# Kernel tuning notes

Hardware: AMD Instinct MI355X
Metric: run time of the kernel (lower is better)

## Reference

```python
import jax, jax.numpy as jnp
import numpy as np

NH = 16      # query heads
NKV = 8      # kv heads
D = 128      # head_dim
HID = 2048   # hidden_size
EPS = 1e-6
THETA = 1e6


def _rmsnorm(x, w, eps=EPS):
    # x: [..., D]; per-head RMSNorm as in Qwen3 q_norm/k_norm
    var = jnp.mean(x * x, axis=-1, keepdims=True)
    return x * jax.lax.rsqrt(var + eps) * w


def _rope(positions, x, theta=THETA):
    # neox-style rotary (sglang get_rope default), rotary_dim == head_dim
    # x: [T, H, D]
    half = D // 2
    inv_freq = 1.0 / (theta ** (jnp.arange(half, dtype=jnp.float32) / half))
    ang = positions.astype(jnp.float32)[:, None] * inv_freq[None, :]   # [T, half]
    cos = jnp.cos(ang)[:, None, :]
    sin = jnp.sin(ang)[:, None, :]
    x1, x2 = x[..., :half], x[..., half:]
    return jnp.concatenate([x1 * cos - x2 * sin, x2 * cos + x1 * sin], axis=-1)


def setup_inputs() -> dict:
    key = jax.random.key(0)
    k1, k2, k3 = jax.random.split(key, 3)
    T = 2048
    return {
        "positions": jnp.arange(T, dtype=jnp.int32),
        "hidden_states": jax.random.normal(k1, (T, HID), dtype=jnp.float32),
        "w_qkv": jax.random.normal(k2, (HID, (NH + 2 * NKV) * D), dtype=jnp.float32) * 0.02,
        "q_norm_w": jnp.ones((D,), dtype=jnp.float32),
        "k_norm_w": jnp.ones((D,), dtype=jnp.float32),
        "w_o": jax.random.normal(k3, (NH * D, HID), dtype=jnp.float32) * 0.02,
    }


def reference(positions, hidden_states, w_qkv, q_norm_w, k_norm_w, w_o):
    T = hidden_states.shape[0]
    q_size, kv_size = NH * D, NKV * D
    qkv = hidden_states @ w_qkv                              # [T, q+2kv]
    q = qkv[:, :q_size].reshape(T, NH, D)
    k = qkv[:, q_size:q_size + kv_size].reshape(T, NKV, D)
    v = qkv[:, q_size + kv_size:].reshape(T, NKV, D)
    q = _rmsnorm(q, q_norm_w)
    k = _rmsnorm(k, k_norm_w)
    q = _rope(positions, q)
    k = _rope(positions, k)
    group = NH // NKV
    k_rep = jnp.repeat(k, group, axis=1)                     # [T, NH, D]
    v_rep = jnp.repeat(v, group, axis=1)
    scale = D ** -0.5
    scores = jnp.einsum('qhd,khd->hqk', q, k_rep) * scale    # [NH, T, T]
    causal = jnp.arange(T)[None, :] <= jnp.arange(T)[:, None]  # [q, k]
    scores = jnp.where(causal[None, :, :], scores, jnp.finfo(scores.dtype).min)
    probs = jax.nn.softmax(scores, axis=-1)
    attn = jnp.einsum('hqk,khd->qhd', probs, v_rep).reshape(T, NH * D)
    return attn @ w_o
```

## Files before the change

### kernel.cpp

```cpp
#include <hip/hip_runtime.h>
#include <cstdint>
#include <cstddef>


#define C_NH 16
#define C_NKV 8
#define C_DH 128
#define C_HID 2048
#define C_NQKV 4096
#define KVB 64

typedef unsigned short u16;
typedef __attribute__((ext_vector_type(8))) short short8;
typedef __attribute__((ext_vector_type(4))) float f32x4;

__device__ __forceinline__ u16 f2bf(float x) {
  uint32_t u = __float_as_uint(x);
  u += 0x7FFFu + ((u >> 16) & 1u);
  return (u16)(u >> 16);
}
__device__ __forceinline__ float bf2f(u16 h) {
  return __uint_as_float(((uint32_t)h) << 16);
}
__device__ __forceinline__ void bsplit(float x, u16& hi, u16& lo) {
  u16 h = f2bf(x);
  hi = h;
  lo = f2bf(x - bf2f(h));
}

__device__ __forceinline__ void gload16(const void* g, void* l) {
  __builtin_amdgcn_global_load_lds(
      (const __attribute__((address_space(1))) void*)g,
      (__attribute__((address_space(3))) void*)l, 16, 0, 0);
}

__global__ void k_trig(const int* __restrict__ pos, float2* __restrict__ tab) {
  int t = blockIdx.x;
  int j = threadIdx.x;
  float inv = 1.0f / powf(1.0e6f, (float)j * (1.0f / 64.0f));
  float ang = (float)pos[t] * inv;
  tab[t * 64 + j] = make_float2(cosf(ang), sinf(ang));
}

struct __align__(8) U4 { u16 a, b, c, d; };

__global__ void k_split(const float* __restrict__ in, u16* __restrict__ hi,
                        u16* __restrict__ lo, int n) {
  int i = (blockIdx.x * 256 + threadIdx.x) * 4;
  if (i >= n) return;
  float4 x = *(const float4*)(in + i);
  U4 hv, lv;
  bsplit(x.x, hv.a, lv.a);
  bsplit(x.y, hv.b, lv.b);
  bsplit(x.z, hv.c, lv.c);
  bsplit(x.w, hv.d, lv.d);
  *(U4*)(hi + i) = hv;
  *(U4*)(lo + i) = lv;
}

__global__ void k_split_tr(const float* __restrict__ in, u16* __restrict__ hi,
                           u16* __restrict__ lo, int K, int N) {
  __shared__ float t[64][65];
  const int kb = blockIdx.y * 64, nb = blockIdx.x * 64;
  const int tid = threadIdx.x;
  for (int i = tid; i < 4096; i += 256) {
    int r = i >> 6, c = i & 63;
    t[r][c] = in[(size_t)(kb + r) * N + nb + c];
  }
  __syncthreads();
  for (int i = tid; i < 4096; i += 256) {
    int r = i >> 6, c = i & 63;
    u16 h, l;
    bsplit(t[c][r], h, l);
    size_t o = (size_t)(nb + r) * K + kb + c;
    hi[o] = h;
    lo[o] = l;
  }
}

__global__ __launch_bounds__(256, 2)
void k_gemm_x3(const u16* __restrict__ Ah, const u16* __restrict__ Al,
               const u16* __restrict__ Bh, const u16* __restrict__ Bl,
               float* __restrict__ C, int M, int N, int K) {
  __shared__ u16 lds[4][4096];
  const int tid = threadIdx.x;
  const int lane = tid & 63;
  const int wv = tid >> 6;
  const int wr = wv >> 1, wc = wv & 1;
  const int mb = blockIdx.y * 128, nb = blockIdx.x * 128;
  const int ra = lane & 15, ko = (lane >> 4) * 8;

  f32x4 acc[4][4] = {};
  const int nk = K >> 5;
  const int rS = lane >> 2, cS = (lane & 3) * 8;

  for (int kt = 0; kt < nk; ++kt) {
    const int kb = kt * 32;
    __syncthreads();
#pragma unroll
    for (int ci = 0; ci < 2; ++ci) {
      int c = wv * 2 + ci;
      int row = c * 16 + rS;
      gload16(Ah + (size_t)(mb + row) * K + kb + cS, &lds[0][c * 512]);
      gload16(Al + (size_t)(mb + row) * K + kb + cS, &lds[1][c * 512]);
      gload16(Bh + (size_t)(nb + row) * K + kb + cS, &lds[2][c * 512]);
      gload16(Bl + (size_t)(nb + row) * K + kb + cS, &lds[3][c * 512]);
    }
    __syncthreads();

    short8 a_h[4], a_l[4], b_h[4], b_l[4];
#pragma unroll
    for (int m = 0; m < 4; ++m) {
      int r = (wr * 64 + m * 16 + ra) * 32 + ko;
      a_h[m] = *(const short8*)&lds[0][r];
      a_l[m] = *(const short8*)&lds[1][r];
    }
#pragma unroll
    for (int n = 0; n < 4; ++n) {
      int r = (wc * 64 + n * 16 + ra) * 32 + ko;
      b_h[n] = *(const short8*)&lds[2][r];
      b_l[n] = *(const short8*)&lds[3][r];
    }
#pragma unroll
    for (int m = 0; m < 4; ++m)
#pragma unroll
      for (int n = 0; n < 4; ++n) {
        acc[m][n] = __builtin_amdgcn_mfma_f32_16x16x32_bf16(a_h[m], b_h[n], acc[m][n], 0, 0, 0);
        acc[m][n] = __builtin_amdgcn_mfma_f32_16x16x32_bf16(a_h[m], b_l[n], acc[m][n], 0, 0, 0);
        acc[m][n] = __builtin_amdgcn_mfma_f32_16x16x32_bf16(a_l[m], b_h[n], acc[m][n], 0, 0, 0);
      }
  }
  const int cr = mb + wr * 64 + (lane >> 4) * 4;
  const int cc = nb + wc * 64 + ra;
#pragma unroll
  for (int m = 0; m < 4; ++m)
#pragma unroll
    for (int n = 0; n < 4; ++n)
#pragma unroll
      for (int r = 0; r < 4; ++r)
        C[(size_t)(cr + m * 16 + r) * N + cc + n * 16] = acc[m][n][r];
}

__global__ void k_normrope(const float* __restrict__ qkv, const float2* __restrict__ tab,
                           const float* __restrict__ qw, const float* __restrict__ kw,
                           u16* __restrict__ Qh, u16* __restrict__ Ql,
                           u16* __restrict__ Kh, u16* __restrict__ Kl,
                           u16* __restrict__ Vh, u16* __restrict__ Vl, int T) {
  int gw = blockIdx.x * 4 + (threadIdx.x >> 6);
  if (gw >= T * 32) return;
  int lane = threadIdx.x & 63;
  int t = gw >> 5, hd = gw & 31;
  const float* src;
  if (hd < C_NH)              src = qkv + (size_t)t * C_NQKV + hd * C_DH;
  else if (hd < C_NH + C_NKV) src = qkv + (size_t)t * C_NQKV + C_NH * C_DH + (hd - C_NH) * C_DH;
  else                        src = qkv + (size_t)t * C_NQKV + (C_NH + C_NKV) * C_DH + (hd - C_NH - C_NKV) * C_DH;
  float x1 = src[lane], x2 = src[lane + 64];

  if (hd >= C_NH + C_NKV) {
    int vh = hd - C_NH - C_NKV;
    u16 h, l;
    bsplit(x1, h, l);
    size_t o1 = ((size_t)vh * C_DH + lane) * T + t;
    Vh[o1] = h; Vl[o1] = l;
    bsplit(x2, h, l);
    size_t o2 = ((size_t)vh * C_DH + lane + 64) * T + t;
    Vh[o2] = h; Vl[o2] = l;
    return;
  }
  float ss = x1 * x1 + x2 * x2;
  ss += __shfl_xor(ss, 1, 64);
  ss += __shfl_xor(ss, 2, 64);
  ss += __shfl_xor(ss, 4, 64);
  ss += __shfl_xor(ss, 8, 64);
  ss += __shfl_xor(ss, 16, 64);
  ss += __shfl_xor(ss, 32, 64);
  float rms = rsqrtf(ss * (1.0f / 128.0f) + 1e-6f);
  const float* w = (hd < C_NH) ? qw : kw;
  float y1 = x1 * rms * w[lane];
  float y2 = x2 * rms * w[lane + 64];
  float2 cs = tab[t * 64 + lane];
  float o1 = y1 * cs.x - y2 * cs.y;
  float o2 = y2 * cs.x + y1 * cs.y;
  u16 h, l;
  if (hd < C_NH) {
    size_t o = ((size_t)t * C_NH + hd) * C_DH + lane;
    bsplit(o1, h, l); Qh[o] = h; Ql[o] = l;
    bsplit(o2, h, l); Qh[o + 64] = h; Ql[o + 64] = l;
  } else {
    int kh = hd - C_NH;
    size_t o = ((size_t)t * C_NKV + kh) * C_DH + lane;
    bsplit(o1, h, l); Kh[o] = h; Kl[o] = l;
    bsplit(o2, h, l); Kh[o + 64] = h; Kl[o + 64] = l;
  }
}

__global__ __launch_bounds__(512, 2)
void k_flash(const u16* __restrict__ Qh, const u16* __restrict__ Ql,
             const u16* __restrict__ Kg_h, const u16* __restrict__ Kg_l,
             const u16* __restrict__ Vg_h, const u16* __restrict__ Vg_l,
             u16* __restrict__ Oh, u16* __restrict__ Ol, int T) {
  __shared__ u16 KV[2][4][KVB * C_DH];
  __shared__ u16 Pex[8][2][16 * 36];
  const int tid = threadIdx.x, lane = tid & 63, wv = tid >> 6;
  const int lm = lane & 15, lq = lane >> 4;
  const int hk = blockIdx.x & 7, qt = blockIdx.x >> 3;
  const int wq = wv & 3, wh = wv >> 2;
  const int h = hk * 2 + wh;
  const int row16 = qt * 64 + wq * 16;

  short8 qfh[4], qfl[4];
#pragma unroll
  for (int kc = 0; kc < 4; ++kc) {
    size_t o = ((size_t)(row16 + lm) * C_NH + h) * C_DH + kc * 32 + lq * 8;
    qfh[kc] = *(const short8*)(Qh + o);
    qfl[kc] = *(const short8*)(Ql + o);
  }
  f32x4 o_acc[8] = {};
  float m_r[4], l_r[4];
#pragma unroll
  for (int r = 0; r < 4; ++r) { m_r[r] = -1e30f; l_r[r] = 0.f; }

  const int s_arr = wv >> 1, s_hf = wv & 1;
  const int s_rr = lane >> 4, s_ph = lane & 15;
  auto stage = [&](int buf, int kt) {
    const int kvb = kt * KVB;
#pragma unroll
    for (int j = 0; j < 8; ++j) {
      const int r0 = s_hf * 32 + j * 4;
      const int r = r0 + s_rr;
      const int c = s_ph ^ (r & 15);
      const u16* g;
      if (s_arr < 2) {
        const u16* base = (s_arr == 0) ? Kg_h : Kg_l;
        g = base + ((size_t)(kvb + r) * C_NKV + hk) * C_DH + c * 8;
      } else {
        const int d = r + ((c >> 3) << 6);
        const u16* base = (s_arr == 2) ? Vg_h : Vg_l;
        g = base + ((size_t)hk * C_DH + d) * T + kvb + (c & 7) * 8;
      }
      gload16(g, &KV[buf][s_arr][r0 * C_DH]);
    }
  };

  const float scale = 0.08838834764831845f;
  const int ntiles = qt + 1;

  stage(0, 0);
  __syncthreads();

  for (int kt = 0; kt < ntiles; ++kt) {
    const int buf = kt & 1;
    const int kvb = kt * KVB;
    if (kt + 1 < ntiles) stage(buf ^ 1, kt + 1);

    f32x4 s[4] = {};
#pragma unroll
    for (int nt = 0; nt < 4; ++nt) {
      const int krow = nt * 16 + lm;
#pragma unroll
      for (int kc = 0; kc < 4; ++kc) {
        const int phys = (kc * 4 + lq) ^ lm;
        short8 bh = *(const short8*)&KV[buf][0][krow * C_DH + phys * 8];
        short8 bl = *(const short8*)&KV[buf][1][krow * C_DH + phys * 8];
        s[nt] = __builtin_amdgcn_mfma_f32_16x16x32_bf16(qfh[kc], bh, s[nt], 0, 0, 0);
        s[nt] = __builtin_amdgcn_mfma_f32_16x16x32_bf16(qfh[kc], bl, s[nt], 0, 0, 0);
        s[nt] = __builtin_amdgcn_mfma_f32_16x16x32_bf16(qfl[kc], bh, s[nt], 0, 0, 0);
      }
    }

    float p[4][4];
#pragma unroll
    for (int r = 0; r < 4; ++r) {
      const int qrow = row16 + lq * 4 + r;
      float sv[4];
#pragma unroll
      for (int nt = 0; nt < 4; ++nt)
        sv[nt] = (kvb + nt * 16 + lm <= qrow) ? s[nt][r] * scale : -1e30f;
      float pm = fmaxf(fmaxf(sv[0], sv[1]), fmaxf(sv[2], sv[3]));
      pm = fmaxf(pm, __shfl_xor(pm, 1, 16));
      pm = fmaxf(pm, __shfl_xor(pm, 2, 16));
      pm = fmaxf(pm, __shfl_xor(pm, 4, 16));
      pm = fmaxf(pm, __shfl_xor(pm, 8, 16));
      float mn = fmaxf(m_r[r], pm);
      float alpha = __expf(m_r[r] - mn);
      float ps = 0.f;
#pragma unroll
      for (int nt = 0; nt < 4; ++nt) { p[nt][r] = __expf(sv[nt] - mn); ps += p[nt][r]; }
      ps += __shfl_xor(ps, 1, 16);
      ps += __shfl_xor(ps, 2, 16);
      ps += __shfl_xor(ps, 4, 16);
      ps += __shfl_xor(ps, 8, 16);
      l_r[r] = l_r[r] * alpha + ps;
      m_r[r] = mn;
#pragma unroll
      for (int jb = 0; jb < 8; ++jb) o_acc[jb][r] *= alpha;
    }

#pragma unroll
    for (int half = 0; half < 2; ++half) {
#pragma unroll
      for (int r = 0; r < 4; ++r)
#pragma unroll
        for (int t2 = 0; t2 < 2; ++t2) {
          u16 ph, pl;
          bsplit(p[half * 2 + t2][r], ph, pl);
          Pex[wv][0][(lq * 4 + r) * 36 + t2 * 16 + lm] = ph;
          Pex[wv][1][(lq * 4 + r) * 36 + t2 * 16 + lm] = pl;
        }
      short8 pah = *(const short8*)&Pex[wv][0][lm * 36 + lq * 8];
      short8 pal = *(const short8*)&Pex[wv][1][lm * 36 + lq * 8];
#pragma unroll
      for (int jb = 0; jb < 8; ++jb) {
        const int phys = (((jb >> 2) << 3) + half * 4 + lq) ^ lm;
        const int roff = ((jb * 16 + lm) & 63) * C_DH + phys * 8;
        short8 vh = *(const short8*)&KV[buf][2][roff];
        short8 vl = *(const short8*)&KV[buf][3][roff];
        o_acc[jb] = __builtin_amdgcn_mfma_f32_16x16x32_bf16(pah, vh, o_acc[jb], 0, 0, 0);
        o_acc[jb] = __builtin_amdgcn_mfma_f32_16x16x32_bf16(pah, vl, o_acc[jb], 0, 0, 0);
        o_acc[jb] = __builtin_amdgcn_mfma_f32_16x16x32_bf16(pal, vh, o_acc[jb], 0, 0, 0);
      }
    }
    __syncthreads();
  }

#pragma unroll
  for (int r = 0; r < 4; ++r) {
    float inv = 1.0f / l_r[r];
    int qrow = row16 + lq * 4 + r;
#pragma unroll
    for (int jb = 0; jb < 8; ++jb) {
      float val = o_acc[jb][r] * inv;
      u16 hh, ll;
      bsplit(val, hh, ll);
      size_t oo = ((size_t)qrow * C_NH + h) * C_DH + jb * 16 + lm;
      Oh[oo] = hh;
      Ol[oo] = ll;
    }
  }
}

extern "C" void kernel_launch(void* const* d_in, const int* in_sizes, int n_in,
                              void* d_out, int out_size, void* d_ws, size_t ws_size,
                              hipStream_t stream) {
  const int*   pos  = (const int*)d_in[0];
  const float* hid  = (const float*)d_in[1];
  const float* wqkv = (const float*)d_in[2];
  const float* qnw  = (const float*)d_in[3];
  const float* knw  = (const float*)d_in[4];
  const float* wo   = (const float*)d_in[5];
  float* out = (float*)d_out;
  const int T = in_sizes[0];

  char* ws = (char*)d_ws;
  const size_t MB = 1024 * 1024;
  u16*    hid_h = (u16*)(ws);
  u16*    hid_l = (u16*)(ws + 8 * MB);
  u16*    wq_h  = (u16*)(ws + 16 * MB);
  u16*    wq_l  = (u16*)(ws + 32 * MB);
  u16*    wo_h  = (u16*)(ws + 48 * MB);
  u16*    wo_l  = (u16*)(ws + 56 * MB);
  float*  qkv   = (float*)(ws + 64 * MB);
  u16*    q_h   = (u16*)(ws + 96 * MB);
  u16*    q_l   = (u16*)(ws + 104 * MB);
  u16*    k_h   = (u16*)(ws + 112 * MB);
  u16*    k_l   = (u16*)(ws + 116 * MB);
  u16*    v_h   = (u16*)(ws + 120 * MB);
  u16*    v_l   = (u16*)(ws + 124 * MB);
  u16*    at_h  = (u16*)(ws + 128 * MB);
  u16*    at_l  = (u16*)(ws + 136 * MB);
  float2* tab   = (float2*)(ws + 144 * MB);

  k_trig<<<T, 64, 0, stream>>>(pos, tab);
  k_split<<<(T * C_HID) / 1024, 256, 0, stream>>>(hid, hid_h, hid_l, T * C_HID);
  k_split_tr<<<dim3(C_NQKV / 64, C_HID / 64), 256, 0, stream>>>(wqkv, wq_h, wq_l, C_HID, C_NQKV);
  k_split_tr<<<dim3(C_HID / 64, C_HID / 64), 256, 0, stream>>>(wo, wo_h, wo_l, C_HID, C_HID);
  k_gemm_x3<<<dim3(C_NQKV / 128, T / 128), 256, 0, stream>>>(
      hid_h, hid_l, wq_h, wq_l, qkv, T, C_NQKV, C_HID);
  k_normrope<<<(T * 32) / 4, 256, 0, stream>>>(qkv, tab, qnw, knw, q_h, q_l, k_h, k_l, v_h, v_l, T);
  k_flash<<<T / 64 * C_NKV, 512, 0, stream>>>(q_h, q_l, k_h, k_l, v_h, v_l, at_h, at_l, T);
  k_gemm_x3<<<dim3(C_HID / 128, T / 128), 256, 0, stream>>>(
      at_h, at_l, wo_h, wo_l, out, T, C_HID, C_HID);
}
```

Measured before the change: 510.1 us.

## Split flash attention KV range three ways and merge partials in a new kernel

The flash kernel now splits each query tile's causal KV range into three chunks. Each chunk runs in its own block and writes unnormalized partial outputs plus row max and sum, and a new merge kernel combines them. The goal is to fix the causal load imbalance and the low block count (256 blocks) on a large GPU. To fit more resident blocks, the KV tile shrinks to 32 rows and double buffering is dropped. This costs extra partial-output traffic, a separate merge launch, and less overlap between loads and compute within each block.

```diff
diff --git a/kernel.cpp b/kernel.cpp
--- a/kernel.cpp
+++ b/kernel.cpp
@@ -8,7 +8,7 @@
 #define C_DH 128
 #define C_HID 2048
 #define C_NQKV 4096
-#define KVB 64
+#define KVB 32
 
 typedef unsigned short u16;
 typedef __attribute__((ext_vector_type(8))) short short8;
@@ -194,16 +194,18 @@
   }
 }
 
-__global__ __launch_bounds__(512, 2)
+__global__ __launch_bounds__(512, 6)
 void k_flash(const u16* __restrict__ Qh, const u16* __restrict__ Ql,
              const u16* __restrict__ Kg_h, const u16* __restrict__ Kg_l,
              const u16* __restrict__ Vg_h, const u16* __restrict__ Vg_l,
-             u16* __restrict__ Oh, u16* __restrict__ Ol, int T) {
-  __shared__ u16 KV[2][4][KVB * C_DH];
+             u16* __restrict__ Oph, u16* __restrict__ Opl,
+             float* __restrict__ Mp, float* __restrict__ Lp, int T) {
+  __shared__ u16 KV[4][KVB * C_DH];
   __shared__ u16 Pex[8][2][16 * 36];
   const int tid = threadIdx.x, lane = tid & 63, wv = tid >> 6;
   const int lm = lane & 15, lq = lane >> 4;
-  const int hk = blockIdx.x & 7, qt = blockIdx.x >> 3;
+  const int f = blockIdx.x;
+  const int hk = f & 7, qt = (f >> 3) & 31, ks = f >> 8;
   const int wq = wv & 3, wh = wv >> 2;
   const int h = hk * 2 + wh;
   const int row16 = qt * 64 + wq * 16;
@@ -222,11 +224,11 @@
 
   const int s_arr = wv >> 1, s_hf = wv & 1;
   const int s_rr = lane >> 4, s_ph = lane & 15;
-  auto stage = [&](int buf, int kt) {
+  auto stage = [&](int kt) {
     const int kvb = kt * KVB;
 #pragma unroll
-    for (int j = 0; j < 8; ++j) {
-      const int r0 = s_hf * 32 + j * 4;
+    for (int j = 0; j < 4; ++j) {
+      const int r0 = s_hf * 16 + j * 4;
       const int r = r0 + s_rr;
       const int c = s_ph ^ (r & 15);
       const u16* g;
@@ -234,58 +236,60 @@
         const u16* base = (s_arr == 0) ? Kg_h : Kg_l;
         g = base + ((size_t)(kvb + r) * C_NKV + hk) * C_DH + c * 8;
       } else {
-        const int d = r + ((c >> 3) << 6);
+        const int d = r + ((c >> 2) << 5);
         const u16* base = (s_arr == 2) ? Vg_h : Vg_l;
-        g = base + ((size_t)hk * C_DH + d) * T + kvb + (c & 7) * 8;
+        g = base + ((size_t)hk * C_DH + d) * T + kvb + (c & 3) * 8;
       }
-      gload16(g, &KV[buf][s_arr][r0 * C_DH]);
+      gload16(g, &KV[s_arr][r0 * C_DH]);
     }
   };
 
   const float scale = 0.08838834764831845f;
-  const int ntiles = qt + 1;
-
-  stage(0, 0);
-  __syncthreads();
-
-  for (int kt = 0; kt < ntiles; ++kt) {
-    const int buf = kt & 1;
+  const int nt32 = 2 * qt + 2;
+  const int t0 = (ks * nt32) / 3, t1 = ((ks + 1) * nt32) / 3;
+
+  for (int kt = t0; kt < t1; ++kt) {
     const int kvb = kt * KVB;
-    if (kt + 1 < ntiles) stage(buf ^ 1, kt + 1);
-
-    f32x4 s[4] = {};
-#pragma unroll
-    for (int nt = 0; nt < 4; ++nt) {
+    stage(kt);
+    __syncthreads();
+
+    f32x4 s[2] = {};
+#pragma unroll
+    for (int nt = 0; nt < 2; ++nt) {
       const int krow = nt * 16 + lm;
 #pragma unroll
       for (int kc = 0; kc < 4; ++kc) {
         const int phys = (kc * 4 + lq) ^ lm;
-        short8 bh = *(const short8*)&KV[buf][0][krow * C_DH + phys * 8];
-        short8 bl = *(const short8*)&KV[buf][1][krow * C_DH + phys * 8];
+        short8 bh = *(const short8*)&KV[0][krow * C_DH + phys * 8];
+        short8 bl = *(const short8*)&KV[1][krow * C_DH + phys * 8];
         s[nt] = __builtin_amdgcn_mfma_f32_16x16x32_bf16(qfh[kc], bh, s[nt], 0, 0, 0);
         s[nt] = __builtin_amdgcn_mfma_f32_16x16x32_bf16(qfh[kc], bl, s[nt], 0, 0, 0);
         s[nt] = __builtin_amdgcn_mfma_f32_16x16x32_bf16(qfl[kc], bh, s[nt], 0, 0, 0);
       }
     }
 
-    float p[4][4];
+    float p[2][4];
 #pragma unroll
     for (int r = 0; r < 4; ++r) {
       const int qrow = row16 + lq * 4 + r;
-      float sv[4];
-#pragma unroll
-      for (int nt = 0; nt < 4; ++nt)
+      float sv[2];
+#pragma unroll
+      for (int nt = 0; nt < 2; ++nt)
         sv[nt] = (kvb + nt * 16 + lm <= qrow) ? s[nt][r] * scale : -1e30f;
-      float pm = fmaxf(fmaxf(sv[0], sv[1]), fmaxf(sv[2], sv[3]));
+      float pm = fmaxf(sv[0], sv[1]);
       pm = fmaxf(pm, __shfl_xor(pm, 1, 16));
       pm = fmaxf(pm, __shfl_xor(pm, 2, 16));
       pm = fmaxf(pm, __shfl_xor(pm, 4, 16));
       pm = fmaxf(pm, __shfl_xor(pm, 8, 16));
       float mn = fmaxf(m_r[r], pm);
+      const float safe = (mn <= -1e29f) ? 0.f : 1.f;
       float alpha = __expf(m_r[r] - mn);
       float ps = 0.f;
 #pragma unroll
-      for (int nt = 0; nt < 4; ++nt) { p[nt][r] = __expf(sv[nt] - mn); ps += p[nt][r]; }
+      for (int nt = 0; nt < 2; ++nt) {
+        p[nt][r] = safe * __expf(sv[nt] - mn);
+        ps += p[nt][r];
+      }
       ps += __shfl_xor(ps, 1, 16);
       ps += __shfl_xor(ps, 2, 16);
       ps += __shfl_xor(ps, 4, 16);
@@ -297,46 +301,76 @@
     }
 
 #pragma unroll
-    for (int half = 0; half < 2; ++half) {
-#pragma unroll
-      for (int r = 0; r < 4; ++r)
-#pragma unroll
-        for (int t2 = 0; t2 < 2; ++t2) {
-          u16 ph, pl;
-          bsplit(p[half * 2 + t2][r], ph, pl);
-          Pex[wv][0][(lq * 4 + r) * 36 + t2 * 16 + lm] = ph;
-          Pex[wv][1][(lq * 4 + r) * 36 + t2 * 16 + lm] = pl;
-        }
-      short8 pah = *(const short8*)&Pex[wv][0][lm * 36 + lq * 8];
-      short8 pal = *(const short8*)&Pex[wv][1][lm * 36 + lq * 8];
-#pragma unroll
-      for (int jb = 0; jb < 8; ++jb) {
-        const int phys = (((jb >> 2) << 3) + half * 4 + lq) ^ lm;
-        const int roff = ((jb * 16 + lm) & 63) * C_DH + phys * 8;
-        short8 vh = *(const short8*)&KV[buf][2][roff];
-        short8 vl = *(const short8*)&KV[buf][3][roff];
-        o_acc[jb] = __builtin_amdgcn_mfma_f32_16x16x32_bf16(pah, vh, o_acc[jb], 0, 0, 0);
-        o_acc[jb] = __builtin_amdgcn_mfma_f32_16x16x32_bf16(pah, vl, o_acc[jb], 0, 0, 0);
-        o_acc[jb] = __builtin_amdgcn_mfma_f32_16x16x32_bf16(pal, vh, o_acc[jb], 0, 0, 0);
+    for (int r = 0; r < 4; ++r)
+#pragma unroll
+      for (int t2 = 0; t2 < 2; ++t2) {
+        u16 ph, pl;
+        bsplit(p[t2][r], ph, pl);
+        Pex[wv][0][(lq * 4 + r) * 36 + t2 * 16 + lm] = ph;
+        Pex[wv][1][(lq * 4 + r) * 36 + t2 * 16 + lm] = pl;
       }
+    short8 pah = *(const short8*)&Pex[wv][0][lm * 36 + lq * 8];
+    short8 pal = *(const short8*)&Pex[wv][1][lm * 36 + lq * 8];
+#pragma unroll
+    for (int jb = 0; jb < 8; ++jb) {
+      const int vrow = (jb & 1) * 16 + lm;
+      const int phys = ((jb >> 1) * 4 + lq) ^ lm;
+      const int roff = vrow * C_DH + phys * 8;
+      short8 vh = *(const short8*)&KV[2][roff];
+      short8 vl = *(const short8*)&KV[3][roff];
+      o_acc[jb] = __builtin_amdgcn_mfma_f32_16x16x32_bf16(pah, vh, o_acc[jb], 0, 0, 0);
+      o_acc[jb] = __builtin_amdgcn_mfma_f32_16x16x32_bf16(pah, vl, o_acc[jb], 0, 0, 0);
+      o_acc[jb] = __builtin_amdgcn_mfma_f32_16x16x32_bf16(pal, vh, o_acc[jb], 0, 0, 0);
     }
     __syncthreads();
   }
 
+  const int S = T * C_NH;
 #pragma unroll
   for (int r = 0; r < 4; ++r) {
-    float inv = 1.0f / l_r[r];
-    int qrow = row16 + lq * 4 + r;
+    const int qrow = row16 + lq * 4 + r;
+    const int rh = qrow * C_NH + h;
+    if (lm == 0) { Mp[ks * S + rh] = m_r[r]; Lp[ks * S + rh] = l_r[r]; }
 #pragma unroll
     for (int jb = 0; jb < 8; ++jb) {
-      float val = o_acc[jb][r] * inv;
       u16 hh, ll;
-      bsplit(val, hh, ll);
-      size_t oo = ((size_t)qrow * C_NH + h) * C_DH + jb * 16 + lm;
-      Oh[oo] = hh;
-      Ol[oo] = ll;
-    }
-  }
+      bsplit(o_acc[jb][r], hh, ll);
+      size_t oo = ((size_t)ks * S + rh) * C_DH + jb * 16 + lm;
+      Oph[oo] = hh;
+      Opl[oo] = ll;
+    }
+  }
+}
+
+__global__ void k_merge(const u16* __restrict__ Oph, const u16* __restrict__ Opl,
+                        const float* __restrict__ Mp, const float* __restrict__ Lp,
+                        u16* __restrict__ Oh, u16* __restrict__ Ol, int T) {
+  const int idx = blockIdx.x * 256 + threadIdx.x;
+  const int rh = idx >> 4, dg = idx & 15;
+  const int S = T * C_NH;
+  float m0 = Mp[rh], m1 = Mp[S + rh], m2 = Mp[2 * S + rh];
+  float M = fmaxf(fmaxf(m0, m1), m2);
+  float w0 = __expf(m0 - M), w1 = __expf(m1 - M), w2 = __expf(m2 - M);
+  float L = w0 * Lp[rh] + w1 * Lp[S + rh] + w2 * Lp[2 * S + rh];
+  float inv = 1.0f / L;
+  const size_t b = (size_t)rh * C_DH + dg * 8;
+  const size_t SO = (size_t)S * C_DH;
+  short8 h0 = *(const short8*)(Oph + b),      l0 = *(const short8*)(Opl + b);
+  short8 h1 = *(const short8*)(Oph + SO + b), l1 = *(const short8*)(Opl + SO + b);
+  short8 h2 = *(const short8*)(Oph + 2 * SO + b), l2 = *(const short8*)(Opl + 2 * SO + b);
+  short8 oh, ol;
+#pragma unroll
+  for (int j = 0; j < 8; ++j) {
+    float o = w0 * (bf2f((u16)h0[j]) + bf2f((u16)l0[j]))
+            + w1 * (bf2f((u16)h1[j]) + bf2f((u16)l1[j]))
+            + w2 * (bf2f((u16)h2[j]) + bf2f((u16)l2[j]));
+    u16 hh, ll;
+    bsplit(o * inv, hh, ll);
+    oh[j] = (short)hh;
+    ol[j] = (short)ll;
+  }
+  *(short8*)(Oh + b) = oh;
+  *(short8*)(Ol + b) = ol;
 }
 
 extern "C" void kernel_launch(void* const* d_in, const int* in_sizes, int n_in,
@@ -369,6 +403,10 @@
   u16*    at_h  = (u16*)(ws + 128 * MB);
   u16*    at_l  = (u16*)(ws + 136 * MB);
   float2* tab   = (float2*)(ws + 144 * MB);
+  u16*   Oph = (u16*)(ws + 16 * MB);
+  float* Mp  = (float*)(ws + 42 * MB);
+  float* Lp  = (float*)(ws + 43 * MB);
+  u16*   Opl = (u16*)(ws + 64 * MB);
 
   k_trig<<<T, 64, 0, stream>>>(pos, tab);
   k_split<<<(T * C_HID) / 1024, 256, 0, stream>>>(hid, hid_h, hid_l, T * C_HID);
@@ -377,7 +415,9 @@
   k_gemm_x3<<<dim3(C_NQKV / 128, T / 128), 256, 0, stream>>>(
       hid_h, hid_l, wq_h, wq_l, qkv, T, C_NQKV, C_HID);
   k_normrope<<<(T * 32) / 4, 256, 0, stream>>>(qkv, tab, qnw, knw, q_h, q_l, k_h, k_l, v_h, v_l, T);
-  k_flash<<<T / 64 * C_NKV, 512, 0, stream>>>(q_h, q_l, k_h, k_l, v_h, v_l, at_h, at_l, T);
+  k_flash<<<3 * T / 64 * C_NKV, 512, 0, stream>>>(q_h, q_l, k_h, k_l, v_h, v_l,
+                                                  Oph, Opl, Mp, Lp, T);
+  k_merge<<<(T * C_NH * 16) / 256, 256, 0, stream>>>(Oph, Opl, Mp, Lp, at_h, at_l, T);
   k_gemm_x3<<<dim3(C_HID / 128, T / 128), 256, 0, stream>>>(
       at_h, at_l, wo_h, wo_l, out, T, C_HID, C_HID);
 }
```

New measurement: 872.6 us. 1.71x slower.
